# Kernel tuning notes

Hardware: AMD Instinct MI355X
Metric: run time of the kernel (lower is better)

## Reference

```python
import jax, jax.numpy as jnp
import numpy as np

B, T, E, H, A, V = 32, 128, 256, 512, 256, 32000
S_SRC, S_CUE = 64, 64
OUT_IN = E + 2 * H + 2 * H  # emb + rnn_out + knowledge + src_ctx + cue_ctx (memory_size=H)
NEG = -1e9


def setup_inputs() -> dict:
    key = jax.random.key(0)
    ks = jax.random.split(key, 20)
    s = lambda k, sh: (jax.random.normal(k, sh) / np.sqrt(sh[0])).astype(jnp.float32)
    inp = {}
    inp['tokens'] = jax.random.randint(ks[0], (B, T), 0, V)
    inp['lengths'] = jax.random.randint(ks[1], (B,), 1, T + 1)
    inp['hidden0'] = jax.random.normal(ks[2], (B, H)) * 0.1
    inp['knowledge'] = jax.random.normal(ks[3], (B, H)) * 0.1
    inp['src_mem'] = jax.random.normal(ks[4], (B, S_SRC, H)) * 0.1
    inp['src_lengths'] = jax.random.randint(ks[5], (B,), 1, S_SRC + 1)
    inp['cue_mem'] = jax.random.normal(ks[6], (B, S_CUE, H)) * 0.1
    inp['cue_lengths'] = jax.random.randint(ks[7], (B,), 1, S_CUE + 1)
    # parameters
    inp['emb'] = jax.random.normal(ks[8], (V, E)) * 0.02
    inp['w_ih'] = s(ks[9], (E, 3 * H)); inp['w_hh'] = s(ks[10], (H, 3 * H))
    inp['b_ih'] = jnp.zeros((3 * H,)); inp['b_hh'] = jnp.zeros((3 * H,))
    Q = E + 2 * H
    inp['src_wq'] = s(ks[11], (Q, A)); inp['src_bq'] = jnp.zeros((A,))
    inp['src_wm'] = s(ks[12], (H, A)); inp['src_v'] = s(ks[13], (A,))
    inp['cue_wq'] = s(ks[14], (Q, A)); inp['cue_bq'] = jnp.zeros((A,))
    inp['cue_wm'] = s(ks[15], (H, A)); inp['cue_v'] = s(ks[16], (A,))
    inp['w_out1'] = s(ks[17], (OUT_IN, H)); inp['b_out1'] = jnp.zeros((H,))
    inp['w_out2'] = s(ks[18], (H, V)); inp['b_out2'] = jnp.zeros((V,))
    return inp


def _mlp_attn(q, mk, mem, wq, bq, v, mask):
    # q: (B,Q), mk = mem@wm precomputed: (B,S,A), mem: (B,S,H), mask: (B,S) True=valid
    scores = jnp.einsum('bsa,a->bs', jnp.tanh((q @ wq + bq)[:, None, :] + mk), v)
    scores = jnp.where(mask, scores, NEG)
    w = jax.nn.softmax(scores, axis=-1)
    return jnp.einsum('bs,bsh->bh', w, mem)


def reference(tokens, lengths, hidden0, knowledge, src_mem, src_lengths, cue_mem,
              cue_lengths, emb, w_ih, w_hh, b_ih, b_hh, src_wq, src_bq, src_wm,
              src_v, cue_wq, cue_bq, cue_wm, cue_v, w_out1, b_out1, w_out2, b_out2):
    x_all = emb[tokens]                                   # (B,T,E) teacher-forced embeddings
    valid = jnp.arange(T)[None, :] < lengths[:, None]     # (B,T)
    src_mask = jnp.arange(S_SRC)[None, :] < src_lengths[:, None]
    cue_mask = jnp.arange(S_CUE)[None, :] < cue_lengths[:, None]
    src_mk = src_mem @ src_wm                             # (B,S,A) hoisted memory projection
    cue_mk = cue_mem @ cue_wm

    def step(h, xs):
        x, vm = xs                                        # (B,E), (B,)
        gi = x @ w_ih + b_ih
        gh = h @ w_hh + b_hh
        i_r, i_z, i_n = jnp.split(gi, 3, axis=-1)
        h_r, h_z, h_n = jnp.split(gh, 3, axis=-1)
        r = jax.nn.sigmoid(i_r + h_r)
        z = jax.nn.sigmoid(i_z + h_z)
        n = jnp.tanh(i_n + r * h_n)
        h_new = (1.0 - z) * n + z * h                     # torch GRU cell
        q = jnp.concatenate([x, h, knowledge], axis=-1)   # query uses OLD hidden (as in source)
        src_ctx = _mlp_attn(q, src_mk, src_mem, src_wq, src_bq, src_v, src_mask)
        cue_ctx = _mlp_attn(q, cue_mk, cue_mem, cue_wq, cue_bq, cue_v, cue_mask)
        out_in = jnp.concatenate([x, h_new, knowledge, src_ctx, cue_ctx], axis=-1)
        vmc = vm[:, None]
        h_next = jnp.where(vmc, h_new, h)                 # only valid rows advance (length-sorted loop)
        return h_next, (jnp.where(vmc, out_in, 0.0), jnp.where(vmc, h_new, 0.0))

    h_final, (out_inputs, hid_mem) = jax.lax.scan(
        step, hidden0, (x_all.transpose(1, 0, 2), valid.T))
    out_inputs = out_inputs.transpose(1, 0, 2)            # (B,T,OUT_IN)
    hidden_memory = hid_mem.transpose(1, 0, 2)            # (B,T,H)
    logits = (out_inputs @ w_out1 + b_out1) @ w_out2 + b_out2
    log_probs = jax.nn.log_softmax(logits, axis=-1)       # (B,T,V)
    return log_probs, hidden_memory, h_final
```

## Files before the change

kernel.cpp:

```cpp
#include <hip/hip_runtime.h>

typedef unsigned int uint;
typedef unsigned short ushort;
using short8 = __attribute__((ext_vector_type(8))) short;
using f32x4  = __attribute__((ext_vector_type(4))) float;

#define DEVFN __device__ __forceinline__

constexpr int B_ = 32, T_ = 128, E_ = 256, H_ = 512, A_ = 256, V_ = 32000, S_ = 64;
constexpr int G3_ = 3 * H_;
constexpr int OUTIN_ = E_ + 4 * H_;
constexpr int M_ = B_ * T_;

DEVFN ushort f2b(float f) {
  uint u = __float_as_uint(f);
  u += 0x7fffu + ((u >> 16) & 1u);
  return (ushort)(u >> 16);
}
DEVFN float b2f(ushort b) { return __uint_as_float(((uint)b) << 16); }
DEVFN float sigmoid_f(float x) { return 1.f / (1.f + __expf(-x)); }
DEVFN float tanh_f(float x) { float e = __expf(2.f * x); return 1.f - 2.f / (e + 1.f); }

__global__ __launch_bounds__(256) void transpose_k(const float* __restrict__ in,
                                                   ushort* __restrict__ out, int R, int C) {
  __shared__ __align__(16) ushort tile[64][65];
  int c0 = blockIdx.x * 64, r0 = blockIdx.y * 64;
  int tx = threadIdx.x & 63, ty = threadIdx.x >> 6;
#pragma unroll
  for (int k = 0; k < 16; k++) {
    int i = ty + k * 4;
    int r = r0 + i, c = c0 + tx;
    if (r < R && c < C) tile[tx][i] = f2b(in[(size_t)r * C + c]);
  }
  __syncthreads();
#pragma unroll
  for (int k = 0; k < 16; k++) {
    int j = ty + k * 4;
    int c = c0 + j, r = r0 + tx;
    if (r < R && c < C) out[(size_t)c * R + r] = tile[j][tx];
  }
}

__global__ void convert_k(const float* __restrict__ in, ushort* __restrict__ out, int n) {
  int i = blockIdx.x * 256 + threadIdx.x;
  if (i < n) out[i] = f2b(in[i]);
}

__global__ __launch_bounds__(256) void gather_k(const int* __restrict__ tokens,
                                                const float* __restrict__ emb,
                                                ushort* __restrict__ xbf) {
  int r = blockIdx.x;
  int t = r >> 5, b = r & 31;
  int tok = tokens[b * T_ + t];
  xbf[(size_t)r * E_ + threadIdx.x] = f2b(emb[(size_t)tok * E_ + threadIdx.x]);
}

__global__ __launch_bounds__(256) void kq_k(const float* __restrict__ knowledge,
                                            const float* __restrict__ wq,
                                            const float* __restrict__ bq,
                                            float* __restrict__ kq) {
  int b = blockIdx.x, a = threadIdx.x;
  const float* kn = knowledge + b * H_;
  float s = 0.f;
  for (int h = 0; h < H_; h++) s += kn[h] * wq[(size_t)(E_ + H_ + h) * A_ + a];
  kq[b * A_ + a] = s + bq[a];
}

template <int OUTBF, int PERM, int HASBIAS>
__global__ __launch_bounds__(256) void gemm_bt(const ushort* __restrict__ Ag,
                                               const ushort* __restrict__ Btg,
                                               const float* __restrict__ bias,
                                               void* __restrict__ Cg, int M, int N, int K) {
  __shared__ __align__(16) ushort Ash[128][40];
  __shared__ __align__(16) ushort Bsh[128][40];
  const int nbx = gridDim.x;
  const int nwg = nbx * gridDim.y;
  const int lin = blockIdx.y * nbx + blockIdx.x;
  const int cpx = nwg >> 3;
  const int swz = (lin & 7) * cpx + (lin >> 3);
  const int m0 = (swz / nbx) * 128, n0 = (swz % nbx) * 128;
  const int tid = threadIdx.x;
  const int wave = tid >> 6, lane = tid & 63, lr = lane & 15, lg = lane >> 4;
  const int wr = wave >> 1, wc = wave & 1;
  f32x4 acc[4][4] = {};
  for (int kk = 0; kk < K; kk += 32) {
    {
      int r = tid >> 2, q = tid & 3;
      *(short8*)&Ash[r][q * 8] = *(const short8*)&Ag[(size_t)(m0 + r) * K + kk + q * 8];
      *(short8*)&Bsh[r][q * 8] = *(const short8*)&Btg[(size_t)(n0 + r) * K + kk + q * 8];
      r += 64;
      *(short8*)&Ash[r][q * 8] = *(const short8*)&Ag[(size_t)(m0 + r) * K + kk + q * 8];
      *(short8*)&Bsh[r][q * 8] = *(const short8*)&Btg[(size_t)(n0 + r) * K + kk + q * 8];
    }
    __syncthreads();
    short8 af[4], bfr[4];
#pragma unroll
    for (int mi = 0; mi < 4; mi++) af[mi] = *(const short8*)&Ash[wr * 64 + mi * 16 + lr][lg * 8];
#pragma unroll
    for (int ni = 0; ni < 4; ni++) bfr[ni] = *(const short8*)&Bsh[wc * 64 + ni * 16 + lr][lg * 8];
#pragma unroll
    for (int mi = 0; mi < 4; mi++)
#pragma unroll
      for (int ni = 0; ni < 4; ni++)
        acc[mi][ni] = __builtin_amdgcn_mfma_f32_16x16x32_bf16(af[mi], bfr[ni], acc[mi][ni], 0, 0, 0);
    __syncthreads();
  }
#pragma unroll
  for (int mi = 0; mi < 4; mi++)
#pragma unroll
    for (int ni = 0; ni < 4; ni++) {
      int col = n0 + wc * 64 + ni * 16 + lr;
      float bv = HASBIAS ? bias[col] : 0.f;
#pragma unroll
      for (int r = 0; r < 4; r++) {
        int row = m0 + wr * 64 + mi * 16 + lg * 4 + r;
        int orow = PERM ? ((row & 31) << 7) + (row >> 5) : row;
        float v = acc[mi][ni][r] + bv;
        if (OUTBF == 1)      ((ushort*)Cg)[(size_t)orow * N + col] = f2b(v);
        else if (OUTBF == 2) ((ushort*)Cg)[(size_t)orow * 2 * N + col] = f2b(v);
        else                 ((float*)Cg)[(size_t)orow * N + col] = v;
      }
    }
}

__global__ void inith_k(const float* __restrict__ h0, ushort* __restrict__ hpb) {
  int g = blockIdx.x * 256 + threadIdx.x;
  hpb[g] = f2b(h0[g]);
}

__global__ __launch_bounds__(128, 1) void scan_k(
    const float* __restrict__ w_hh, const float* __restrict__ b_hh,
    const float* __restrict__ gi, const int* __restrict__ lengths,
    const float* __restrict__ h0, ushort* hpb,
    float* __restrict__ hidmem, float* __restrict__ hfinal, uint* flags) {
  __shared__ __align__(16) ushort pk[2][16][16];
  const int wg = blockIdx.x;
  const int c0 = wg * 16;
  const int tid = threadIdx.x;
  const int wave = tid >> 6, lane = tid & 63, lr = lane & 15, lg = lane >> 4;
  const int c = c0 + lr;

  short8 wf0[16], wf1[16], wf2[16];
#pragma unroll
  for (int kk = 0; kk < 16; kk++) {
    short8 v0, v1, v2;
#pragma unroll
    for (int i = 0; i < 8; i++) {
      int k = kk * 32 + lg * 8 + i;
      v0[i] = (short)f2b(w_hh[(size_t)k * G3_ + 0 * H_ + c]);
      v1[i] = (short)f2b(w_hh[(size_t)k * G3_ + 1 * H_ + c]);
      v2[i] = (short)f2b(w_hh[(size_t)k * G3_ + 2 * H_ + c]);
    }
    wf0[kk] = v0; wf1[kk] = v1; wf2[kk] = v2;
  }
  const float bh0 = b_hh[c], bh1 = b_hh[H_ + c], bh2 = b_hh[2 * H_ + c];
  int len[4];
  float hp[4];
#pragma unroll
  for (int r = 0; r < 4; r++) {
    int bt = 16 * wave + lg * 4 + r;
    len[r] = lengths[bt];
    hp[r] = h0[(size_t)bt * H_ + c];
  }

#pragma unroll 1
  for (int t = 0; t < T_; t++) {
    float g0[4], g1[4], g2[4];
#pragma unroll
    for (int r = 0; r < 4; r++) {
      int bt = 16 * wave + lg * 4 + r;
      const float* gr = gi + (size_t)(t * 32 + bt) * G3_ + c;
      g0[r] = gr[0]; g1[r] = gr[H_]; g2[r] = gr[2 * H_];
    }
    if (t > 0) {
      while (true) {
        uint f = __hip_atomic_load(&flags[lane * 32], __ATOMIC_RELAXED, __HIP_MEMORY_SCOPE_AGENT);
        if (__all((int)(f >= (uint)t))) break;
        __builtin_amdgcn_s_sleep(1);
      }
    }
    asm volatile("" ::: "memory");

    const ushort* Sb = hpb + (size_t)t * (B_ * H_);
    const int rowA = 16 * wave + lr;
    f32x4 a0 = {}, a1 = {}, a2 = {};
#pragma unroll
    for (int kk = 0; kk < 16; kk++) {
      short8 av = *(const short8*)(Sb + rowA * H_ + kk * 32 + lg * 8);
      a0 = __builtin_amdgcn_mfma_f32_16x16x32_bf16(av, wf0[kk], a0, 0, 0, 0);
      a1 = __builtin_amdgcn_mfma_f32_16x16x32_bf16(av, wf1[kk], a1, 0, 0, 0);
      a2 = __builtin_amdgcn_mfma_f32_16x16x32_bf16(av, wf2[kk], a2, 0, 0, 0);
    }

    ushort* Un16 = hpb + (size_t)(t + 1) * (B_ * H_);
    float hmv[4];
#pragma unroll
    for (int r = 0; r < 4; r++) {
      float rr = sigmoid_f(g0[r] + a0[r] + bh0);
      float zz = sigmoid_f(g1[r] + a1[r] + bh1);
      float nn = tanh_f(g2[r] + rr * (a2[r] + bh2));
      float hv = (1.f - zz) * nn + zz * hp[r];
      bool valid = t < len[r];
      float hx = valid ? hv : hp[r];
      hp[r] = hx;
      hmv[r] = valid ? hv : 0.f;
      pk[wave][lg * 4 + r][lr] = f2b(hx);
    }
    if (lane < 32) {
      int row = lane >> 1, half = lane & 1;
      short8 v = *(const short8*)&pk[wave][row][half * 8];
      ushort* gp = Un16 + ((size_t)(16 * wave + row) * H_ + c0 + half * 8);
      asm volatile("global_store_dwordx4 %0, %1, off sc1" :: "v"(gp), "v"(v) : "memory");
    }
    asm volatile("s_waitcnt vmcnt(0)" ::: "memory");
    if (lane == 0)
      __hip_atomic_store(&flags[(wg * 2 + wave) * 32], (uint)(t + 1),
                         __ATOMIC_RELAXED, __HIP_MEMORY_SCOPE_AGENT);
#pragma unroll
    for (int r = 0; r < 4; r++) {
      int bt = 16 * wave + lg * 4 + r;
      hidmem[((size_t)bt * T_ + t) * H_ + c] = hmv[r];
    }
  }
#pragma unroll
  for (int r = 0; r < 4; r++) {
    int bt = 16 * wave + lg * 4 + r;
    hfinal[(size_t)bt * H_ + c] = hp[r];
  }
}

__global__ __launch_bounds__(256) void attn_k(
    const float* __restrict__ qxk, const float* __restrict__ qh, const float* __restrict__ kq,
    const float* __restrict__ mk, const float* __restrict__ mem, const float* __restrict__ vvec,
    const int* __restrict__ slen, float* __restrict__ ctx) {
  __shared__ float qf[A_], vv[A_], sc[S_];
  int bx = blockIdx.x;
  int b = bx >> 7, t = bx & 127;
  int row = t * B_ + b;
  int tid = threadIdx.x;
  qf[tid] = qxk[(size_t)row * A_ + tid] + qh[(size_t)row * A_ + tid] + kq[b * A_ + tid];
  vv[tid] = vvec[tid];
  __syncthreads();
  int s = tid >> 2, q4 = tid & 3;
  const float* mkr = mk + ((size_t)(b * S_) + s) * A_;
  float part = 0.f;
#pragma unroll 4
  for (int i = 0; i < 64; i++) {
    int a = q4 + (i << 2);
    part += tanh_f(qf[a] + mkr[a]) * vv[a];
  }
  part += __shfl_xor(part, 1, 64);
  part += __shfl_xor(part, 2, 64);
  if (q4 == 0) sc[s] = part;
  __syncthreads();
  if (tid < S_) {
    float v = (tid < slen[b]) ? sc[tid] : -1e9f;
    float mm = v;
    for (int off = 1; off < 64; off <<= 1) mm = fmaxf(mm, __shfl_xor(mm, off, 64));
    float e = __expf(v - mm);
    float ss = e;
    for (int off = 1; off < 64; off <<= 1) ss += __shfl_xor(ss, off, 64);
    sc[tid] = e / ss;
  }
  __syncthreads();
  float c0 = 0.f, c1 = 0.f;
  const float* mb = mem + (size_t)b * S_ * H_;
  for (int ss2 = 0; ss2 < S_; ss2++) {
    float w = sc[ss2];
    c0 += w * mb[ss2 * H_ + tid];
    c1 += w * mb[ss2 * H_ + tid + 256];
  }
  ctx[(size_t)row * H_ + tid] = c0;
  ctx[(size_t)row * H_ + tid + 256] = c1;
}

__global__ __launch_bounds__(256) void assemble_k(
    const ushort* __restrict__ xbf, const float* __restrict__ hm,
    const float* __restrict__ knowledge, const float* __restrict__ ctxs,
    const float* __restrict__ ctxc, const int* __restrict__ lengths,
    ushort* __restrict__ outin) {
  int r = blockIdx.x;
  int t = r >> 5, b = r & 31;
  bool valid = t < lengths[b];
  int tid = threadIdx.x;
  ushort* dst = outin + (size_t)r * OUTIN_;
#pragma unroll
  for (int kblk = 0; kblk < 9; kblk++) {
    int i = kblk * 256 + tid;
    ushort v;
    if (i < E_)               v = xbf[(size_t)r * E_ + i];
    else if (i < E_ + H_)     v = f2b(hm[((size_t)b * T_ + t) * H_ + i - E_]);
    else if (i < E_ + 2 * H_) v = f2b(knowledge[b * H_ + i - (E_ + H_)]);
    else if (i < E_ + 3 * H_) v = f2b(ctxs[(size_t)r * H_ + i - (E_ + 2 * H_)]);
    else                      v = f2b(ctxc[(size_t)r * H_ + i - (E_ + 3 * H_)]);
    dst[i] = valid ? v : (ushort)0;
  }
}

__global__ __launch_bounds__(256) void logsoftmax_k(float* __restrict__ logits) {
  __shared__ float redm[4], reds[4];
  float* row = logits + (size_t)blockIdx.x * V_;
  const short8* rg = (const short8*)row;
  const int tid = threadIdx.x;
  short8 buf[16];
  float m = -3.4e38f, s = 0.f;
#pragma unroll
  for (int k = 0; k < 16; k++) {
    int i = tid + k * 256;
    if (i < V_ / 8) {
      short8 v = rg[i];
      buf[k] = v;
      float f0 = b2f((ushort)v[0]), f1 = b2f((ushort)v[1]);
      float f2 = b2f((ushort)v[2]), f3 = b2f((ushort)v[3]);
      float f4 = b2f((ushort)v[4]), f5 = b2f((ushort)v[5]);
      float f6 = b2f((ushort)v[6]), f7 = b2f((ushort)v[7]);
      float vm = fmaxf(fmaxf(fmaxf(f0, f1), fmaxf(f2, f3)),
                       fmaxf(fmaxf(f4, f5), fmaxf(f6, f7)));
      float nm = fmaxf(m, vm);
      s = s * __expf(m - nm) + __expf(f0 - nm) + __expf(f1 - nm) + __expf(f2 - nm) +
          __expf(f3 - nm) + __expf(f4 - nm) + __expf(f5 - nm) + __expf(f6 - nm) +
          __expf(f7 - nm);
      m = nm;
    }
  }
  for (int off = 1; off < 64; off <<= 1) {
    float om = __shfl_xor(m, off, 64), os = __shfl_xor(s, off, 64);
    float nm = fmaxf(m, om);
    s = s * __expf(m - nm) + os * __expf(om - nm);
    m = nm;
  }
  if ((tid & 63) == 0) { redm[tid >> 6] = m; reds[tid >> 6] = s; }
  __syncthreads();
  float M = fmaxf(fmaxf(redm[0], redm[1]), fmaxf(redm[2], redm[3]));
  float S = reds[0] * __expf(redm[0] - M) + reds[1] * __expf(redm[1] - M) +
            reds[2] * __expf(redm[2] - M) + reds[3] * __expf(redm[3] - M);
  float lse = M + __logf(S);
  __syncthreads();
#pragma unroll
  for (int k = 0; k < 16; k++) {
    int i = tid + k * 256;
    if (i < V_ / 8) {
      short8 v = buf[k];
      float4 o0, o1;
      o0.x = b2f((ushort)v[0]) - lse; o0.y = b2f((ushort)v[1]) - lse;
      o0.z = b2f((ushort)v[2]) - lse; o0.w = b2f((ushort)v[3]) - lse;
      o1.x = b2f((ushort)v[4]) - lse; o1.y = b2f((ushort)v[5]) - lse;
      o1.z = b2f((ushort)v[6]) - lse; o1.w = b2f((ushort)v[7]) - lse;
      *(float4*)&row[i * 8] = o0;
      *(float4*)&row[i * 8 + 4] = o1;
    }
  }
}

extern "C" void kernel_launch(void* const* d_in, const int* in_sizes, int n_in,
                              void* d_out, int out_size, void* d_ws, size_t ws_size,
                              hipStream_t stream) {
  const int*   tokens    = (const int*)  d_in[0];
  const int*   lengths   = (const int*)  d_in[1];
  const float* hidden0   = (const float*)d_in[2];
  const float* knowledge = (const float*)d_in[3];
  const float* src_mem   = (const float*)d_in[4];
  const int*   src_len   = (const int*)  d_in[5];
  const float* cue_mem   = (const float*)d_in[6];
  const int*   cue_len   = (const int*)  d_in[7];
  const float* emb       = (const float*)d_in[8];
  const float* w_ih      = (const float*)d_in[9];
  const float* w_hh      = (const float*)d_in[10];
  const float* b_ih      = (const float*)d_in[11];
  const float* b_hh      = (const float*)d_in[12];
  const float* src_wq    = (const float*)d_in[13];
  const float* src_bq    = (const float*)d_in[14];
  const float* src_wm    = (const float*)d_in[15];
  const float* src_v     = (const float*)d_in[16];
  const float* cue_wq    = (const float*)d_in[17];
  const float* cue_bq    = (const float*)d_in[18];
  const float* cue_wm    = (const float*)d_in[19];
  const float* cue_v     = (const float*)d_in[20];
  const float* w_out1    = (const float*)d_in[21];
  const float* b_out1    = (const float*)d_in[22];
  const float* w_out2    = (const float*)d_in[23];
  const float* b_out2    = (const float*)d_in[24];

  float* out_lp = (float*)d_out;
  float* out_hm = out_lp + (size_t)M_ * V_;
  float* out_hf = out_hm + (size_t)M_ * H_;

  char* scb = (char*)d_out;
  size_t off = 0;
  auto alloc = [&](size_t bytes) -> void* {
    void* p = scb + off;
    off = (off + bytes + 255) & ~(size_t)255;
    return p;
  };
  float*  GI    = (float*) alloc((size_t)M_ * G3_ * 4);
  float*  QXKs  = (float*) alloc((size_t)M_ * A_ * 4);
  float*  QXKc  = (float*) alloc((size_t)M_ * A_ * 4);
  float*  QHs   = (float*) alloc((size_t)M_ * A_ * 4);
  float*  QHc   = (float*) alloc((size_t)M_ * A_ * 4);
  float*  CTXs  = (float*) alloc((size_t)M_ * H_ * 4);
  float*  CTXc  = (float*) alloc((size_t)M_ * H_ * 4);
  ushort* OUTIN = (ushort*)alloc((size_t)M_ * OUTIN_ * 2);
  ushort* XBF   = (ushort*)alloc((size_t)M_ * E_ * 2);
  ushort* WIHT  = (ushort*)alloc((size_t)G3_ * E_ * 2);
  ushort* WQXTs = (ushort*)alloc((size_t)A_ * E_ * 2);
  ushort* WQXTc = (ushort*)alloc((size_t)A_ * E_ * 2);
  ushort* WQHTs = (ushort*)alloc((size_t)A_ * H_ * 2);
  ushort* WQHTc = (ushort*)alloc((size_t)A_ * H_ * 2);
  ushort* WMTs  = (ushort*)alloc((size_t)A_ * H_ * 2);
  ushort* WMTc  = (ushort*)alloc((size_t)A_ * H_ * 2);
  ushort* WO1T  = (ushort*)alloc((size_t)H_ * OUTIN_ * 2);
  ushort* MEMBs = (ushort*)alloc((size_t)B_ * S_ * H_ * 2);
  ushort* MEMBc = (ushort*)alloc((size_t)B_ * S_ * H_ * 2);
  float*  MKs   = (float*) alloc((size_t)B_ * S_ * A_ * 4);
  float*  MKc   = (float*) alloc((size_t)B_ * S_ * A_ * 4);
  float*  KQs   = (float*) alloc((size_t)B_ * A_ * 4);
  float*  KQc   = (float*) alloc((size_t)B_ * A_ * 4);
  ushort* HPB   = (ushort*)alloc((size_t)(T_ + 1) * B_ * H_ * 2);

  uint* FLAGS = (uint*)d_ws;
  ushort* WO2T = (ushort*)((char*)d_ws + 8192);
  ushort* HID1 = (ushort*)((char*)d_ws + 8192 + (size_t)V_ * H_ * 2);

  dim3 blk(256);
  hipMemsetAsync(FLAGS, 0, 8192, stream);

  transpose_k<<<dim3(G3_ / 64, E_ / 64), blk, 0, stream>>>(w_ih, WIHT, E_, G3_);
  transpose_k<<<dim3(A_ / 64, E_ / 64), blk, 0, stream>>>(src_wq, WQXTs, E_, A_);
  transpose_k<<<dim3(A_ / 64, H_ / 64), blk, 0, stream>>>(src_wq + (size_t)E_ * A_, WQHTs, H_, A_);
  transpose_k<<<dim3(A_ / 64, E_ / 64), blk, 0, stream>>>(cue_wq, WQXTc, E_, A_);
  transpose_k<<<dim3(A_ / 64, H_ / 64), blk, 0, stream>>>(cue_wq + (size_t)E_ * A_, WQHTc, H_, A_);
  transpose_k<<<dim3(A_ / 64, H_ / 64), blk, 0, stream>>>(src_wm, WMTs, H_, A_);
  transpose_k<<<dim3(A_ / 64, H_ / 64), blk, 0, stream>>>(cue_wm, WMTc, H_, A_);
  transpose_k<<<dim3(H_ / 64, OUTIN_ / 64), blk, 0, stream>>>(w_out1, WO1T, OUTIN_, H_);
  transpose_k<<<dim3(V_ / 64, H_ / 64), blk, 0, stream>>>(w_out2, WO2T, H_, V_);
  convert_k<<<(B_ * S_ * H_ + 255) / 256, blk, 0, stream>>>(src_mem, MEMBs, B_ * S_ * H_);
  convert_k<<<(B_ * S_ * H_ + 255) / 256, blk, 0, stream>>>(cue_mem, MEMBc, B_ * S_ * H_);

  gather_k<<<M_, blk, 0, stream>>>(tokens, emb, XBF);
  kq_k<<<B_, blk, 0, stream>>>(knowledge, src_wq, src_bq, KQs);
  kq_k<<<B_, blk, 0, stream>>>(knowledge, cue_wq, cue_bq, KQc);

  gemm_bt<0, 0, 1><<<dim3(G3_ / 128, M_ / 128), blk, 0, stream>>>(XBF, WIHT, b_ih, GI, M_, G3_, E_);
  gemm_bt<0, 0, 0><<<dim3(A_ / 128, M_ / 128), blk, 0, stream>>>(XBF, WQXTs, nullptr, QXKs, M_, A_, E_);
  gemm_bt<0, 0, 0><<<dim3(A_ / 128, M_ / 128), blk, 0, stream>>>(XBF, WQXTc, nullptr, QXKc, M_, A_, E_);
  gemm_bt<0, 0, 0><<<dim3(A_ / 128, (B_ * S_) / 128), blk, 0, stream>>>(MEMBs, WMTs, nullptr, MKs, B_ * S_, A_, H_);
  gemm_bt<0, 0, 0><<<dim3(A_ / 128, (B_ * S_) / 128), blk, 0, stream>>>(MEMBc, WMTc, nullptr, MKc, B_ * S_, A_, H_);

  inith_k<<<(B_ * H_) / 256, blk, 0, stream>>>(hidden0, HPB);
  scan_k<<<32, dim3(128), 0, stream>>>(w_hh, b_hh, GI, lengths, hidden0, HPB, out_hm, out_hf, FLAGS);

  gemm_bt<0, 0, 0><<<dim3(A_ / 128, M_ / 128), blk, 0, stream>>>(HPB, WQHTs, nullptr, QHs, M_, A_, H_);
  gemm_bt<0, 0, 0><<<dim3(A_ / 128, M_ / 128), blk, 0, stream>>>(HPB, WQHTc, nullptr, QHc, M_, A_, H_);
  attn_k<<<M_, blk, 0, stream>>>(QXKs, QHs, KQs, MKs, src_mem, src_v, src_len, CTXs);
  attn_k<<<M_, blk, 0, stream>>>(QXKc, QHc, KQc, MKc, cue_mem, cue_v, cue_len, CTXc);

  assemble_k<<<M_, blk, 0, stream>>>(XBF, out_hm, knowledge, CTXs, CTXc, lengths, OUTIN);
  gemm_bt<1, 0, 1><<<dim3(H_ / 128, M_ / 128), blk, 0, stream>>>(OUTIN, WO1T, b_out1, HID1, M_, H_, OUTIN_);
  gemm_bt<2, 1, 1><<<dim3(V_ / 128, M_ / 128), blk, 0, stream>>>(HID1, WO2T, b_out2, out_lp, M_, V_, H_);
  logsoftmax_k<<<M_, blk, 0, stream>>>(out_lp);
}
```

Baseline: 1.514 ms.

## Use direct global-to-LDS loads in GEMM and per-wave flag polling in GRU

The GEMM tile loads now use global_load_lds, which writes 16-byte chunks straight into LDS without passing through registers, and the padded tiles become unpadded 32-wide layouts. The GRU recurrence's flag spin-wait now has each wave poll a subset of flags indexed by lane and wave, replacing every lane reading lane*32. The first change is meant to cut VGPR traffic and load latency in the dominant GEMMs. Dropping the padding may add LDS bank conflicts on the fragment reads. The flag indexing change alters which producers each wave waits on, which could affect correctness if the flag layout does not match.

```diff
diff --git a/kernel.cpp b/kernel.cpp
--- a/kernel.cpp
+++ b/kernel.cpp
@@ -20,6 +20,12 @@
 DEVFN float b2f(ushort b) { return __uint_as_float(((uint)b) << 16); }
 DEVFN float sigmoid_f(float x) { return 1.f / (1.f + __expf(-x)); }
 DEVFN float tanh_f(float x) { float e = __expf(2.f * x); return 1.f - 2.f / (e + 1.f); }
+
+DEVFN void gload_lds16(const ushort* g, ushort* l) {
+  __builtin_amdgcn_global_load_lds(
+      (const __attribute__((address_space(1))) void*)g,
+      (__attribute__((address_space(3))) void*)l, 16, 0, 0);
+}
 
 __global__ __launch_bounds__(256) void transpose_k(const float* __restrict__ in,
                                                    ushort* __restrict__ out, int R, int C) {
@@ -71,8 +77,8 @@
                                                const ushort* __restrict__ Btg,
                                                const float* __restrict__ bias,
                                                void* __restrict__ Cg, int M, int N, int K) {
-  __shared__ __align__(16) ushort Ash[128][40];
-  __shared__ __align__(16) ushort Bsh[128][40];
+  __shared__ __align__(16) ushort Ash[128 * 32];
+  __shared__ __align__(16) ushort Bsh[128 * 32];
   const int nbx = gridDim.x;
   const int nwg = nbx * gridDim.y;
   const int lin = blockIdx.y * nbx + blockIdx.x;
@@ -82,22 +88,23 @@
   const int tid = threadIdx.x;
   const int wave = tid >> 6, lane = tid & 63, lr = lane & 15, lg = lane >> 4;
   const int wr = wave >> 1, wc = wave & 1;
+  const int rb = lane >> 2, cb = (lane & 3) * 8;
   f32x4 acc[4][4] = {};
   for (int kk = 0; kk < K; kk += 32) {
-    {
-      int r = tid >> 2, q = tid & 3;
-      *(short8*)&Ash[r][q * 8] = *(const short8*)&Ag[(size_t)(m0 + r) * K + kk + q * 8];
-      *(short8*)&Bsh[r][q * 8] = *(const short8*)&Btg[(size_t)(n0 + r) * K + kk + q * 8];
-      r += 64;
-      *(short8*)&Ash[r][q * 8] = *(const short8*)&Ag[(size_t)(m0 + r) * K + kk + q * 8];
-      *(short8*)&Bsh[r][q * 8] = *(const short8*)&Btg[(size_t)(n0 + r) * K + kk + q * 8];
+#pragma unroll
+    for (int j = 0; j < 2; j++) {
+      int blk = wave * 2 + j;
+      gload_lds16(&Ag[(size_t)(m0 + blk * 16 + rb) * K + kk + cb], &Ash[blk * 16 * 32]);
+      gload_lds16(&Btg[(size_t)(n0 + blk * 16 + rb) * K + kk + cb], &Bsh[blk * 16 * 32]);
     }
     __syncthreads();
     short8 af[4], bfr[4];
 #pragma unroll
-    for (int mi = 0; mi < 4; mi++) af[mi] = *(const short8*)&Ash[wr * 64 + mi * 16 + lr][lg * 8];
-#pragma unroll
-    for (int ni = 0; ni < 4; ni++) bfr[ni] = *(const short8*)&Bsh[wc * 64 + ni * 16 + lr][lg * 8];
+    for (int mi = 0; mi < 4; mi++)
+      af[mi] = *(const short8*)&Ash[(wr * 64 + mi * 16 + lr) * 32 + lg * 8];
+#pragma unroll
+    for (int ni = 0; ni < 4; ni++)
+      bfr[ni] = *(const short8*)&Bsh[(wc * 64 + ni * 16 + lr) * 32 + lg * 8];
 #pragma unroll
     for (int mi = 0; mi < 4; mi++)
 #pragma unroll
@@ -163,6 +170,8 @@
     hp[r] = h0[(size_t)bt * H_ + c];
   }
 
+  const uint fidx = ((uint)(lane & 31) * 2 + (uint)wave) * 32;
+
 #pragma unroll 1
   for (int t = 0; t < T_; t++) {
     float g0[4], g1[4], g2[4];
@@ -174,7 +183,7 @@
     }
     if (t > 0) {
       while (true) {
-        uint f = __hip_atomic_load(&flags[lane * 32], __ATOMIC_RELAXED, __HIP_MEMORY_SCOPE_AGENT);
+        uint f = __hip_atomic_load(&flags[fidx], __ATOMIC_RELAXED, __HIP_MEMORY_SCOPE_AGENT);
         if (__all((int)(f >= (uint)t))) break;
         __builtin_amdgcn_s_sleep(1);
       }
```

Measured after the change: 1.537 ms. About the same (+1.5%).
